# Optimization experiments

Hardware: AMD Instinct MI355X
Metric: run time of the kernel (lower is better)

Reference implementation:

```python
import jax, jax.numpy as jnp
import numpy as np

N = 1048576          # number of sample points
C = 32               # feature_dim per plane
PAIRS = ((0, 1), (0, 2), (1, 2))  # itertools.combinations(range(3), 2)


def setup_inputs() -> dict:
    key = jax.random.key(0)
    k0, k1, k2, k3 = jax.random.split(key, 4)
    # grid_sample coords must lie in [-1, 1]
    x = jax.random.uniform(k0, (N, 3), jnp.float32, -1.0, 1.0)
    # torch.nn.init.uniform_ default is U[0, 1)
    planes_128 = jax.random.uniform(k1, (3, C, 128, 128), jnp.float32)
    planes_256 = jax.random.uniform(k2, (3, C, 256, 256), jnp.float32)
    planes_512 = jax.random.uniform(k3, (3, C, 512, 512), jnp.float32)
    return {"x": x, "planes_128": planes_128, "planes_256": planes_256,
            "planes_512": planes_512}


def _bilinear_sample(plane, coords):
    """plane: (C, H, W); coords: (N, 2) in [-1,1], last dim = (x, y).
    Matches torch grid_sample(mode='bilinear', align_corners=True).
    Returns (N, C)."""
    _, H, W = plane.shape
    gx, gy = coords[:, 0], coords[:, 1]
    ix = (gx + 1.0) * 0.5 * (W - 1)   # x indexes width
    iy = (gy + 1.0) * 0.5 * (H - 1)   # y indexes height
    x0f = jnp.clip(jnp.floor(ix), 0.0, W - 1)
    y0f = jnp.clip(jnp.floor(iy), 0.0, H - 1)
    wx = ix - x0f
    wy = iy - y0f
    x0 = x0f.astype(jnp.int32)
    y0 = y0f.astype(jnp.int32)
    x1 = jnp.minimum(x0 + 1, W - 1)
    y1 = jnp.minimum(y0 + 1, H - 1)
    v00 = plane[:, y0, x0]  # (C, N)
    v01 = plane[:, y0, x1]
    v10 = plane[:, y1, x0]
    v11 = plane[:, y1, x1]
    out = (v00 * (1 - wx) * (1 - wy) + v01 * wx * (1 - wy)
           + v10 * (1 - wx) * wy + v11 * wx * wy)  # (C, N)
    return out.T  # (N, C)


def reference(x, planes_128, planes_256, planes_512):
    # coords[p] = x[:, (i, j)] for pair p -> grid (x=dim i, y=dim j)
    coords = jnp.stack([x[:, jnp.array(p)] for p in PAIRS])  # (3, N, 2)
    feats = []
    for planes in (planes_128, planes_256, planes_512):
        sampled = jax.vmap(_bilinear_sample)(planes, coords)  # (3, N, C)
        feats.append(jnp.prod(sampled, axis=0))               # (N, C)
    return jnp.concatenate(feats, axis=-1)  # (N, 96); dropout(p=0) is identity
```

## Files before the change

kernel.cpp:

```cpp
#include <hip/hip_runtime.h>
#include <hip/hip_fp16.h>


constexpr int kN = 1048576;
constexpr int kC = 32;
constexpr int kCells = 32 * 32 * 32;

typedef float f32x4 __attribute__((ext_vector_type(4)));
typedef short s16x4 __attribute__((ext_vector_type(4)));

__global__ __launch_bounds__(1024) void kp_prep(const float* __restrict__ in128,
                                                const float* __restrict__ in256,
                                                const float* __restrict__ in512,
                                                __half* __restrict__ planes,
                                                unsigned* __restrict__ hist) {
    const int tx = threadIdx.x, ty = threadIdx.y;
    const int b = blockIdx.x;
    if (b < 32) {
        hist[b * 1024 + ty * 32 + tx] = 0u;
    }
    const float* in;
    __half* out;
    int R, local;
    if (b < 1536) {
        in = in128; out = planes; R = 128; local = b;
    } else if (b < 1536 + 6144) {
        in = in256; out = planes + (size_t)3 * 128 * 128 * kC; R = 256; local = b - 1536;
    } else {
        in = in512; out = planes + (size_t)3 * 128 * 128 * kC + (size_t)3 * 256 * 256 * kC;
        R = 512; local = b - 1536 - 6144;
    }
    const int xtiles = R / 32;
    const int x0 = (local % xtiles) * 32;
    const int rem = local / xtiles;
    const int y = rem % R;
    const int p = rem / R;
    __shared__ float tile[32][33];
    tile[ty][tx] = in[(((size_t)p * kC + ty) * R + y) * R + x0 + tx];
    __syncthreads();
    out[(((size_t)p * R + y) * R + x0 + ty) * kC + tx] = __float2half_rn(tile[tx][ty]);
}

__device__ __forceinline__ unsigned cell_key(float x, float y, float z) {
    int cx = min(max((int)((x + 1.f) * 16.f), 0), 31);
    int cy = min(max((int)((y + 1.f) * 16.f), 0), 31);
    int cz = min(max((int)((z + 1.f) * 16.f), 0), 31);
    unsigned m = 0;
#pragma unroll
    for (int b = 0; b < 5; ++b) {
        m |= ((unsigned)((cx >> b) & 1)) << (3 * b);
        m |= ((unsigned)((cy >> b) & 1)) << (3 * b + 1);
        m |= ((unsigned)((cz >> b) & 1)) << (3 * b + 2);
    }
    return m;
}

__global__ __launch_bounds__(256) void kp_hist(const float* __restrict__ xs,
                                               unsigned* __restrict__ hist) {
    int n = blockIdx.x * 256 + threadIdx.x;
    float x = xs[n * 3 + 0], y = xs[n * 3 + 1], z = xs[n * 3 + 2];
    atomicAdd(&hist[cell_key(x, y, z)], 1u);
}

__global__ __launch_bounds__(1024) void kp_scan(const unsigned* __restrict__ hist,
                                                unsigned* __restrict__ cursor) {
    __shared__ unsigned sums[1024];
    const int t = threadIdx.x;
    const int per = kCells / 1024;
    unsigned local[32];
    unsigned s = 0;
    const int base = t * per;
#pragma unroll
    for (int i = 0; i < per; ++i) { local[i] = hist[base + i]; s += local[i]; }
    sums[t] = s;
    __syncthreads();
    for (int off = 1; off < 1024; off <<= 1) {
        unsigned v = (t >= off) ? sums[t - off] : 0u;
        __syncthreads();
        sums[t] += v;
        __syncthreads();
    }
    unsigned run = (t == 0) ? 0u : sums[t - 1];
#pragma unroll
    for (int i = 0; i < per; ++i) { cursor[base + i] = run; run += local[i]; }
}

__global__ __launch_bounds__(256) void kp_scatter(const float* __restrict__ xs,
                                                  unsigned* __restrict__ cursor,
                                                  f32x4* __restrict__ sorted) {
    int n = blockIdx.x * 256 + threadIdx.x;
    float x = xs[n * 3 + 0], y = xs[n * 3 + 1], z = xs[n * 3 + 2];
    unsigned pos = atomicAdd(&cursor[cell_key(x, y, z)], 1u);
    f32x4 v = {x, y, z, __uint_as_float((unsigned)n)};
    __builtin_nontemporal_store(v, &sorted[pos]);
}

__device__ __forceinline__ void load4h(const __half* __restrict__ p, float* v) {
    union { s16x4 s; __half2 h[2]; } u;
    u.s = *reinterpret_cast<const s16x4*>(p);
    float2 f01 = __half22float2(u.h[0]);
    float2 f23 = __half22float2(u.h[1]);
    v[0] = f01.x; v[1] = f01.y; v[2] = f23.x; v[3] = f23.y;
}

template<int R>
__device__ __forceinline__ void sample_res(const __half* __restrict__ planes, int c4,
                                           const float* gx, const float* gy, float* f) {
    const float fr = (float)(R - 1);
    f[0] = f[1] = f[2] = f[3] = 1.f;
#pragma unroll
    for (int p = 0; p < 3; ++p) {
        float ix = (gx[p] + 1.f) * 0.5f * fr;
        float iy = (gy[p] + 1.f) * 0.5f * fr;
        float x0f = fminf(fmaxf(floorf(ix), 0.f), fr);
        float y0f = fminf(fmaxf(floorf(iy), 0.f), fr);
        float wx = ix - x0f, wy = iy - y0f;
        int xi0 = (int)x0f, yi0 = (int)y0f;
        int xi1 = min(xi0 + 1, R - 1), yi1 = min(yi0 + 1, R - 1);
        const __half* pl = planes + (size_t)p * R * R * kC + c4;
        float v00[4], v01[4], v10[4], v11[4];
        load4h(pl + (yi0 * R + xi0) * kC, v00);
        load4h(pl + (yi0 * R + xi1) * kC, v01);
        load4h(pl + (yi1 * R + xi0) * kC, v10);
        load4h(pl + (yi1 * R + xi1) * kC, v11);
        float w00 = (1.f - wx) * (1.f - wy), w01 = wx * (1.f - wy);
        float w10 = (1.f - wx) * wy,         w11 = wx * wy;
#pragma unroll
        for (int j = 0; j < 4; ++j)
            f[j] *= w00 * v00[j] + w01 * v01[j] + w10 * v10[j] + w11 * v11[j];
    }
}

__global__ __launch_bounds__(256) void kp_sample_sorted(const f32x4* __restrict__ pts,
                                                        const __half* __restrict__ t128,
                                                        const __half* __restrict__ t256,
                                                        const __half* __restrict__ t512,
                                                        float* __restrict__ out) {
    const int nwg = (kN * 8) / 256;
    int bid = blockIdx.x;
    bid = (bid & 7) * (nwg / 8) + (bid >> 3);
    const int li = threadIdx.x;
    const int n  = bid * 32 + (li >> 3);
    const int c4 = (li & 7) << 2;
    f32x4 pt = pts[n];
    const float a = pt.x, b = pt.y, d = pt.z;
    const unsigned oi = __float_as_uint(pt.w);
    const float gx[3] = {a, a, b};
    const float gy[3] = {b, d, d};
    float* o = out + (size_t)oi * 96 + c4;
    float f[4];
    sample_res<128>(t128, c4, gx, gy, f);
    __builtin_nontemporal_store(f32x4{f[0], f[1], f[2], f[3]}, (f32x4*)o);
    sample_res<256>(t256, c4, gx, gy, f);
    __builtin_nontemporal_store(f32x4{f[0], f[1], f[2], f[3]}, (f32x4*)(o + 32));
    sample_res<512>(t512, c4, gx, gy, f);
    __builtin_nontemporal_store(f32x4{f[0], f[1], f[2], f[3]}, (f32x4*)(o + 64));
}

__global__ __launch_bounds__(256) void kp_sample_f32(const float* __restrict__ xs,
                                                     const float* __restrict__ p128,
                                                     const float* __restrict__ p256,
                                                     const float* __restrict__ p512,
                                                     float* __restrict__ out) {
    const int t = blockIdx.x * 256 + (int)threadIdx.x;
    const int n = t >> 5;
    const int c = t & 31;
    const float a = xs[n * 3 + 0], b = xs[n * 3 + 1], d = xs[n * 3 + 2];
    const float gxs[3] = {a, a, b};
    const float gys[3] = {b, d, d};
    const float* planes[3] = {p128, p256, p512};
    const int Rs[3] = {128, 256, 512};
    float* o = out + (size_t)n * 96;
#pragma unroll
    for (int r = 0; r < 3; ++r) {
        const int R = Rs[r];
        const float fr = (float)(R - 1);
        float f = 1.0f;
#pragma unroll
        for (int p = 0; p < 3; ++p) {
            float ix = (gxs[p] + 1.f) * 0.5f * fr;
            float iy = (gys[p] + 1.f) * 0.5f * fr;
            float x0f = fminf(fmaxf(floorf(ix), 0.f), fr);
            float y0f = fminf(fmaxf(floorf(iy), 0.f), fr);
            float wx = ix - x0f, wy = iy - y0f;
            int xi0 = (int)x0f, yi0 = (int)y0f;
            int xi1 = min(xi0 + 1, R - 1), yi1 = min(yi0 + 1, R - 1);
            const float* pc = planes[r] + ((size_t)p * kC + c) * R * R;
            float v00 = pc[yi0 * R + xi0], v01 = pc[yi0 * R + xi1];
            float v10 = pc[yi1 * R + xi0], v11 = pc[yi1 * R + xi1];
            f *= v00 * (1.f - wx) * (1.f - wy) + v01 * wx * (1.f - wy)
               + v10 * (1.f - wx) * wy + v11 * wx * wy;
        }
        __builtin_nontemporal_store(f, o + r * 32 + c);
    }
}

extern "C" void kernel_launch(void* const* d_in, const int* in_sizes, int n_in,
                              void* d_out, int out_size, void* d_ws, size_t ws_size,
                              hipStream_t stream) {
    const float* xs   = (const float*)d_in[0];
    const float* p128 = (const float*)d_in[1];
    const float* p256 = (const float*)d_in[2];
    const float* p512 = (const float*)d_in[3];
    float* out = (float*)d_out;

    const size_t n128 = (size_t)3 * 128 * 128 * kC;
    const size_t n256 = (size_t)3 * 256 * 256 * kC;
    const size_t n512 = (size_t)3 * 512 * 512 * kC;
    const size_t planes_b = (n128 + n256 + n512) * sizeof(__half);
    const size_t sorted_b = (size_t)kN * 16;
    const size_t hist_b   = (size_t)kCells * 4;
    const size_t need = sorted_b + planes_b + 2 * hist_b + 256;

    const int nblk8 = (kN * 8) / 256;
    const int ntiles = 1536 + 6144 + 24576;

    if (ws_size >= need) {
        f32x4* sorted = (f32x4*)d_ws;
        __half* planes = (__half*)((char*)d_ws + sorted_b);
        __half* t128 = planes;
        __half* t256 = t128 + n128;
        __half* t512 = t256 + n256;
        unsigned* hist   = (unsigned*)((char*)d_ws + sorted_b + planes_b);
        unsigned* cursor = hist + kCells;

        kp_prep<<<ntiles, dim3(32, 32), 0, stream>>>(p128, p256, p512, planes, hist);
        kp_hist<<<kN / 256, 256, 0, stream>>>(xs, hist);
        kp_scan<<<1, 1024, 0, stream>>>(hist, cursor);
        kp_scatter<<<kN / 256, 256, 0, stream>>>(xs, cursor, sorted);
        kp_sample_sorted<<<nblk8, 256, 0, stream>>>(sorted, t128, t256, t512, out);
    } else {
        kp_sample_f32<<<(kN * 32) / 256, 256, 0, stream>>>(xs, p128, p256, p512, out);
    }
}
```

Baseline: 413.3 us.

## Split plane transpose into per-resolution half2 kernels and coarsen spatial sort grid

```diff
diff --git a/kernel.cpp b/kernel.cpp
--- a/kernel.cpp
+++ b/kernel.cpp
@@ -4,55 +4,46 @@
 
 constexpr int kN = 1048576;
 constexpr int kC = 32;
-constexpr int kCells = 32 * 32 * 32;
+constexpr int kCells = 16 * 16 * 16;
 
 typedef float f32x4 __attribute__((ext_vector_type(4)));
 typedef short s16x4 __attribute__((ext_vector_type(4)));
 
-__global__ __launch_bounds__(1024) void kp_prep(const float* __restrict__ in128,
-                                                const float* __restrict__ in256,
-                                                const float* __restrict__ in512,
-                                                __half* __restrict__ planes,
-                                                unsigned* __restrict__ hist) {
-    const int tx = threadIdx.x, ty = threadIdx.y;
-    const int b = blockIdx.x;
-    if (b < 32) {
-        hist[b * 1024 + ty * 32 + tx] = 0u;
-    }
-    const float* in;
-    __half* out;
-    int R, local;
-    if (b < 1536) {
-        in = in128; out = planes; R = 128; local = b;
-    } else if (b < 1536 + 6144) {
-        in = in256; out = planes + (size_t)3 * 128 * 128 * kC; R = 256; local = b - 1536;
-    } else {
-        in = in512; out = planes + (size_t)3 * 128 * 128 * kC + (size_t)3 * 256 * 256 * kC;
-        R = 512; local = b - 1536 - 6144;
-    }
-    const int xtiles = R / 32;
-    const int x0 = (local % xtiles) * 32;
-    const int rem = local / xtiles;
-    const int y = rem % R;
-    const int p = rem / R;
-    __shared__ float tile[32][33];
-    tile[ty][tx] = in[(((size_t)p * kC + ty) * R + y) * R + x0 + tx];
+__global__ __launch_bounds__(1024) void kp_transpose_h2(const float* __restrict__ in,
+                                                        __half2* __restrict__ out, int R) {
+    __shared__ float tile[32][65];
+    const int tid = threadIdx.y * 16 + threadIdx.x;
+    const int rx = tid & 63;
+    const int rc = tid >> 6;
+    const int x0 = blockIdx.x * 64;
+    const int y  = blockIdx.y;
+    const int p  = blockIdx.z;
+    tile[rc][rx]      = in[(((size_t)p * kC + rc) * R + y) * R + x0 + rx];
+    tile[rc + 16][rx] = in[(((size_t)p * kC + rc + 16) * R + y) * R + x0 + rx];
     __syncthreads();
-    out[(((size_t)p * R + y) * R + x0 + ty) * kC + tx] = __float2half_rn(tile[tx][ty]);
+    const int c2 = threadIdx.x;
+    const int xl = threadIdx.y;
+    out[(((size_t)p * R + y) * R + x0 + xl) * 16 + c2] =
+        __floats2half2_rn(tile[2 * c2][xl], tile[2 * c2 + 1][xl]);
 }
 
 __device__ __forceinline__ unsigned cell_key(float x, float y, float z) {
-    int cx = min(max((int)((x + 1.f) * 16.f), 0), 31);
-    int cy = min(max((int)((y + 1.f) * 16.f), 0), 31);
-    int cz = min(max((int)((z + 1.f) * 16.f), 0), 31);
+    int cx = min(max((int)((x + 1.f) * 8.f), 0), 15);
+    int cy = min(max((int)((y + 1.f) * 8.f), 0), 15);
+    int cz = min(max((int)((z + 1.f) * 8.f), 0), 15);
     unsigned m = 0;
 #pragma unroll
-    for (int b = 0; b < 5; ++b) {
+    for (int b = 0; b < 4; ++b) {
         m |= ((unsigned)((cx >> b) & 1)) << (3 * b);
         m |= ((unsigned)((cy >> b) & 1)) << (3 * b + 1);
         m |= ((unsigned)((cz >> b) & 1)) << (3 * b + 2);
     }
     return m;
+}
+
+__global__ __launch_bounds__(256) void kp_zero(unsigned* __restrict__ p, int n) {
+    int i = blockIdx.x * 256 + threadIdx.x;
+    if (i < n) p[i] = 0u;
 }
 
 __global__ __launch_bounds__(256) void kp_hist(const float* __restrict__ xs,
@@ -67,7 +58,7 @@
     __shared__ unsigned sums[1024];
     const int t = threadIdx.x;
     const int per = kCells / 1024;
-    unsigned local[32];
+    unsigned local[per];
     unsigned s = 0;
     const int base = t * per;
 #pragma unroll
@@ -212,8 +203,8 @@
     const size_t hist_b   = (size_t)kCells * 4;
     const size_t need = sorted_b + planes_b + 2 * hist_b + 256;
 
+    dim3 tblk(16, 64);
     const int nblk8 = (kN * 8) / 256;
-    const int ntiles = 1536 + 6144 + 24576;
 
     if (ws_size >= need) {
         f32x4* sorted = (f32x4*)d_ws;
@@ -224,7 +215,10 @@
         unsigned* hist   = (unsigned*)((char*)d_ws + sorted_b + planes_b);
         unsigned* cursor = hist + kCells;
 
-        kp_prep<<<ntiles, dim3(32, 32), 0, stream>>>(p128, p256, p512, planes, hist);
+        kp_transpose_h2<<<dim3(128 / 64, 128, 3), tblk, 0, stream>>>(p128, (__half2*)t128, 128);
+        kp_transpose_h2<<<dim3(256 / 64, 256, 3), tblk, 0, stream>>>(p256, (__half2*)t256, 256);
+        kp_transpose_h2<<<dim3(512 / 64, 512, 3), tblk, 0, stream>>>(p512, (__half2*)t512, 512);
+        kp_zero<<<kCells / 256, 256, 0, stream>>>(hist, kCells);
         kp_hist<<<kN / 256, 256, 0, stream>>>(xs, hist);
         kp_scan<<<1, 1024, 0, stream>>>(hist, cursor);
         kp_scatter<<<kN / 256, 256, 0, stream>>>(xs, cursor, sorted);
```

After: 407.7 us. Within noise of the previous version (-1.4%).
